# Performance work log

Hardware: AMD Instinct MI355X
Metric: run time of the kernel (lower is better)

Reference implementation:

```python
import jax, jax.numpy as jnp
import numpy as np
from jax import lax

NMS_THRESH = 0.5
BN_EPS = 1e-5
TO_REMOVE = 1.0  # neural-motifs box convention (+1 in width/height)


def nms_overlaps(boxes):
    # boxes: [N, C, 4] xyxy -> per-class pairwise IoU [N, N, C]
    x1 = jnp.maximum(boxes[:, None, :, 0], boxes[None, :, :, 0])
    y1 = jnp.maximum(boxes[:, None, :, 1], boxes[None, :, :, 1])
    x2 = jnp.minimum(boxes[:, None, :, 2], boxes[None, :, :, 2])
    y2 = jnp.minimum(boxes[:, None, :, 3], boxes[None, :, :, 3])
    inter = jnp.clip(x2 - x1 + TO_REMOVE, 0.0) * jnp.clip(y2 - y1 + TO_REMOVE, 0.0)
    area = (boxes[:, :, 2] - boxes[:, :, 0] + TO_REMOVE) * (boxes[:, :, 3] - boxes[:, :, 1] + TO_REMOVE)  # [N,C]
    union = area[:, None, :] + area[None, :, :] - inter
    return inter / union


def greedy_nms_labels(obj_dists, is_overlap):
    # faithful port of nms_per_cls: iterative argmax + per-class suppression
    N, C = obj_dists.shape
    scores = jax.nn.softmax(obj_dists, axis=-1)
    scores = scores.at[:, 0].set(-1.0)  # kill background column

    def step(carry, _):
        scores, labels = carry
        flat = jnp.argmax(scores)          # row-major, same as np.unravel_index
        box_ind = flat // C
        cls_ind = flat % C
        labels = labels.at[box_ind].set(cls_ind.astype(jnp.int32))
        ov = is_overlap[box_ind, :, cls_ind]  # [N] bool
        col = jnp.where(ov, 0.0, scores[:, cls_ind])
        scores = scores.at[:, cls_ind].set(col)
        scores = scores.at[box_ind, :].set(-1.0)
        return (scores, labels), None

    (_, labels), _ = lax.scan(step, (scores, jnp.zeros(N, jnp.int32)), None, length=N)
    return labels


def setup_inputs() -> dict:
    key = jax.random.key(0)
    ks = jax.random.split(key, 16)
    N, C, D, E, H, P = 400, 151, 4096, 200, 512, 128
    x = jax.random.normal(ks[0], (N, D), jnp.float32)
    predict_logits = jax.random.normal(ks[1], (N, C), jnp.float32) * 2.0
    pos_input = jax.random.uniform(ks[2], (N, 9), jnp.float32)
    xy = jax.random.uniform(ks[3], (N, C, 2), jnp.float32) * 800.0
    wh = jax.random.uniform(ks[4], (N, C, 2), jnp.float32) * 200.0 + 1.0
    boxes_per_cls = jnp.concatenate([xy, xy + wh], axis=-1)
    sc = lambda k, sh: jax.random.normal(k, sh, jnp.float32) * np.float32(1.0 / np.sqrt(sh[0]))
    return {
        'x': x,
        'predict_logits': predict_logits,
        'pos_input': pos_input,
        'boxes_per_cls': boxes_per_cls,
        'obj_embed_w': jax.random.normal(ks[5], (C, E), jnp.float32) * 0.1,
        'obj_embed2_w': jax.random.normal(ks[6], (C, E), jnp.float32) * 0.1,
        'w_pos1': sc(ks[7], (9, 32)), 'b_pos1': jnp.zeros(32, jnp.float32),
        'bn_gamma': jnp.ones(32, jnp.float32), 'bn_beta': jnp.zeros(32, jnp.float32),
        'bn_mean': jnp.zeros(32, jnp.float32), 'bn_var': jnp.ones(32, jnp.float32),
        'w_pos2': sc(ks[8], (32, P)), 'b_pos2': jnp.zeros(P, jnp.float32),
        'w_lin': sc(ks[9], (D + E + P, H)), 'b_lin': jnp.zeros(H, jnp.float32),
        'w_out': sc(ks[10], (H, C)), 'b_out': jnp.zeros(C, jnp.float32),
        'w_fc': sc(ks[11], (D + E + P, H)), 'b_fc': jnp.zeros(H, jnp.float32),
    }


def reference(x, predict_logits, pos_input, boxes_per_cls, obj_embed_w, obj_embed2_w,
              w_pos1, b_pos1, bn_gamma, bn_beta, bn_mean, bn_var, w_pos2, b_pos2,
              w_lin, b_lin, w_out, b_out, w_fc, b_fc):
    # sgdet inference path of VTransEFeaturePE.forward
    obj_embed = jax.nn.softmax(predict_logits, axis=-1) @ obj_embed_w           # [N,E]
    h = pos_input @ w_pos1 + b_pos1                                             # Linear(9,32)
    h = (h - bn_mean) / jnp.sqrt(bn_var + BN_EPS) * bn_gamma + bn_beta          # BN eval
    pos_embed = jax.nn.relu(h @ w_pos2 + b_pos2)                                # [N,128]
    rep = jnp.concatenate([x, obj_embed, pos_embed], axis=-1)                   # [N,4424]
    obj_dists = (rep @ w_lin + b_lin) @ w_out + b_out                           # [N,C]
    is_overlap = nms_overlaps(boxes_per_cls) >= NMS_THRESH                      # [N,N,C]
    obj_preds = greedy_nms_labels(obj_dists, is_overlap)                        # [N] int32
    obj_embed2 = obj_embed2_w[obj_preds]                                        # [N,E]
    obj_rel_rep = jnp.concatenate([x, pos_embed, obj_embed2], axis=-1)
    edge_ctx = jax.nn.relu(obj_rel_rep @ w_fc + b_fc)                           # [N,H]
    return (obj_dists, obj_preds, edge_ctx)
```

## Files before the change

kernel.cpp:

```cpp
#include <hip/hip_runtime.h>
#include <hip/hip_bf16.h>
#include <stdint.h>

#define NB 400
#define NC 151
#define DX 4096
#define DE 200
#define DP 128
#define DH 512
#define KREP 4424
#define TAILW 328
#define MPAD 416
#define SPLITK 8
#define TILES1 139
#define TILES2 132
#define SKSTRIDE 152

__device__ __forceinline__ uint32_t f2ord(float f) {
  uint32_t u = __float_as_uint(f);
  return (u & 0x80000000u) ? ~u : (u | 0x80000000u);
}

__global__ __launch_bounds__(256) void k_embed(
    const float* __restrict__ logits, const float* __restrict__ obj_embed_w,
    const float* __restrict__ pos_input, const float* __restrict__ w_pos1,
    const float* __restrict__ b_pos1, const float* __restrict__ bn_gamma,
    const float* __restrict__ bn_beta, const float* __restrict__ bn_mean,
    const float* __restrict__ bn_var, const float* __restrict__ w_pos2,
    const float* __restrict__ b_pos2, float* __restrict__ tail1) {
  int r = blockIdx.x, t = threadIdx.x;
  if (r >= NB) {
    if (t < TAILW) tail1[r * TAILW + t] = 0.f;
    return;
  }
  __shared__ float p[NC];
  __shared__ float red[256];
  __shared__ float hb[32];

  float v = (t < NC) ? logits[r * NC + t] : -INFINITY;
  red[t] = v; __syncthreads();
  for (int s = 128; s > 0; s >>= 1) { if (t < s) red[t] = fmaxf(red[t], red[t + s]); __syncthreads(); }
  float m = red[0]; __syncthreads();
  float e = (t < NC) ? expf(v - m) : 0.f;
  red[t] = e; __syncthreads();
  for (int s = 128; s > 0; s >>= 1) { if (t < s) red[t] += red[t + s]; __syncthreads(); }
  float sum = red[0];
  if (t < NC) p[t] = e / sum;

  if (t < 32) {
    float acc = b_pos1[t];
    for (int k = 0; k < 9; k++) acc += pos_input[r * 9 + k] * w_pos1[k * 32 + t];
    acc = (acc - bn_mean[t]) / sqrtf(bn_var[t] + 1e-5f) * bn_gamma[t] + bn_beta[t];
    hb[t] = acc;
  }
  __syncthreads();

  if (t < DE) {
    float acc = 0.f;
    for (int k = 0; k < NC; k++) acc += p[k] * obj_embed_w[k * DE + t];
    tail1[r * TAILW + t] = acc;
  }
  if (t < DP) {
    float acc = b_pos2[t];
    for (int k = 0; k < 32; k++) acc += hb[k] * w_pos2[k * DP + t];
    tail1[r * TAILW + DE + t] = fmaxf(acc, 0.f);
  }
}

__device__ __forceinline__ void gemm_body(
    float (*As)[36], float (*Bs)[68],
    const float* __restrict__ x, const float* __restrict__ tail,
    const float* __restrict__ w, float* __restrict__ part,
    int bid, int tiles, int toff) {
  int tid = threadIdx.x;
  int n0 = (bid & 7) * 64, m0 = ((bid >> 3) % 13) * 32;
  int z = bid / 104;
  int tbeg = (z * tiles) / SPLITK, tend = ((z + 1) * tiles) / SPLITK;
  int ty = tid >> 4, tx = tid & 15;
  int a_r = tid >> 3, a_c = (tid & 7) << 2;
  int b_r = tid >> 4, b_c = (tid & 15) << 2;
  float4 acc0 = {0, 0, 0, 0}, acc1 = {0, 0, 0, 0};

  auto loadA = [&](int t) -> float4 {
    int k = t * 32 + a_c;
    int row = m0 + a_r;
    float4 v = {0, 0, 0, 0};
    if (k < KREP) {
      if (k < DX) { if (row < NB) v = *(const float4*)&x[(size_t)row * DX + k]; }
      else v = *(const float4*)&tail[row * TAILW + toff + (k - DX)];
    }
    return v;
  };
  auto loadB = [&](int t, int roff) -> float4 {
    int k = t * 32 + b_r + roff;
    float4 v = {0, 0, 0, 0};
    if (k < KREP) v = *(const float4*)&w[(size_t)k * DH + n0 + b_c];
    return v;
  };

  float4 pa = loadA(tbeg), pb0 = loadB(tbeg, 0), pb1 = loadB(tbeg, 16);
  for (int t = tbeg; t < tend; t++) {
    __syncthreads();
    *(float4*)&As[a_r][a_c] = pa;
    *(float4*)&Bs[b_r][b_c] = pb0;
    *(float4*)&Bs[b_r + 16][b_c] = pb1;
    __syncthreads();
    if (t + 1 < tend) { pa = loadA(t + 1); pb0 = loadB(t + 1, 0); pb1 = loadB(t + 1, 16); }
#pragma unroll
    for (int k4 = 0; k4 < 8; k4++) {
      float4 a0 = *(float4*)&As[ty * 2][k4 * 4];
      float4 a1 = *(float4*)&As[ty * 2 + 1][k4 * 4];
#pragma unroll
      for (int j = 0; j < 4; j++) {
        float4 bv = *(float4*)&Bs[k4 * 4 + j][tx * 4];
        float av0 = (&a0.x)[j], av1 = (&a1.x)[j];
        acc0.x += av0 * bv.x; acc0.y += av0 * bv.y; acc0.z += av0 * bv.z; acc0.w += av0 * bv.w;
        acc1.x += av1 * bv.x; acc1.y += av1 * bv.y; acc1.z += av1 * bv.z; acc1.w += av1 * bv.w;
      }
    }
  }
  int row0 = m0 + ty * 2, col = n0 + tx * 4;
  float* base = part + (size_t)z * NB * DH;
  if (row0 < NB)     *(float4*)&base[row0 * DH + col] = acc0;
  if (row0 + 1 < NB) *(float4*)&base[(row0 + 1) * DH + col] = acc1;
}

__global__ __launch_bounds__(256) void k_g1ov(
    const float* __restrict__ x, const float* __restrict__ tail1,
    const float* __restrict__ w_lin, float* __restrict__ part,
    const float* __restrict__ boxes, uint64_t* __restrict__ ov_bits) {
  __shared__ __align__(16) float As[32][36];
  __shared__ __align__(16) float Bs[32][68];
  int bid = blockIdx.x;
  if (bid >= 832) {
    int c = bid - 832;
    int t = threadIdx.x;
    __shared__ float4 bx[NB];
    const float4* bp4 = (const float4*)boxes;
    for (int j = t; j < NB; j += 256) bx[j] = bp4[j * NC + c];
    __syncthreads();
    int wave = t >> 6, lane = t & 63;
    for (int b = wave; b < NB; b += 4) {
      float4 A = bx[b];
      float areaA = (A.z - A.x + 1.f) * (A.w - A.y + 1.f);
      for (int chunk = 0; chunk < 7; chunk++) {
        int j = chunk * 64 + lane;
        bool ov = false;
        if (j < NB) {
          float4 B = bx[j];
          float x1 = fmaxf(A.x, B.x), y1 = fmaxf(A.y, B.y);
          float x2 = fminf(A.z, B.z), y2 = fminf(A.w, B.w);
          float iw = fmaxf(x2 - x1 + 1.f, 0.f), ih = fmaxf(y2 - y1 + 1.f, 0.f);
          float inter = iw * ih;
          float areaB = (B.z - B.x + 1.f) * (B.w - B.y + 1.f);
          ov = (inter / (areaA + areaB - inter)) >= 0.5f;
        }
        uint64_t mask = __ballot(ov);
        if (lane == 0) ov_bits[((size_t)(b * NC + c) << 3) + chunk] = mask;
      }
    }
    return;
  }
  gemm_body(As, Bs, x, tail1, w_lin, part, bid, TILES1, 0);
}

__global__ __launch_bounds__(256) void k_dists(
    const float* __restrict__ part, const float* __restrict__ b_lin,
    const float* __restrict__ w_out, const float* __restrict__ b_out,
    float* __restrict__ out_dists, uint64_t* __restrict__ skeys) {
  int r = blockIdx.x, t = threadIdx.x;
  __shared__ float h[DH];
  __shared__ float red[256];
  __shared__ float sval[NC];
  float s0 = b_lin[t], s1 = b_lin[t + 256];
#pragma unroll
  for (int z = 0; z < SPLITK; z++) {
    const float* pr = part + ((size_t)z * NB + r) * DH;
    s0 += pr[t]; s1 += pr[t + 256];
  }
  h[t] = s0; h[t + 256] = s1;
  __syncthreads();

  float acc = -INFINITY;
  if (t < NC) {
    acc = b_out[t];
    for (int k = 0; k < DH; k++) acc += h[k] * w_out[k * NC + t];
    out_dists[r * NC + t] = acc;
  }
  red[t] = (t < NC) ? acc : -INFINITY; __syncthreads();
  for (int s = 128; s > 0; s >>= 1) { if (t < s) red[t] = fmaxf(red[t], red[t + s]); __syncthreads(); }
  float mx = red[0]; __syncthreads();
  float e = (t < NC) ? expf(acc - mx) : 0.f;
  red[t] = e; __syncthreads();
  for (int s = 128; s > 0; s >>= 1) { if (t < s) red[t] += red[t + s]; __syncthreads(); }
  float sum = red[0];
  if (t < NC) sval[t] = e / sum;
  __syncthreads();

  if (t >= 1 && t < NC) {
    float v = sval[t];
    int rank = 0;
    for (int c2 = 1; c2 < NC; c2++) {
      float v2 = sval[c2];
      rank += (v2 > v) || (v2 == v && c2 < t);
    }
    skeys[(size_t)r * SKSTRIDE + rank] =
        ((uint64_t)f2ord(v) << 17) | ((uint64_t)(511 - r) << 8) | (uint64_t)t;
  }
}

struct GemmSm { float As[32][36]; float Bs[32][68]; };
struct NmsSm  { uint64_t top4[2][4][4]; uint64_t amask[8]; uint64_t rmask[8];
                uint32_t rcol32[512]; uint64_t ovc[NB][8]; };

__global__ __launch_bounds__(256) void k_nms_g2a(
    const uint64_t* __restrict__ ov_bits, const uint64_t* __restrict__ skeys,
    int* __restrict__ labels_g, float* __restrict__ out_preds,
    const float* __restrict__ x, const float* __restrict__ tail1,
    const float* __restrict__ w_fc, float* __restrict__ part) {
  __shared__ __align__(16) union { GemmSm g; NmsSm n; } sm;
  if (blockIdx.x > 0) {
    gemm_body(sm.g.As, sm.g.Bs, x, tail1, w_fc, part, blockIdx.x - 1, TILES2, DE);
    return;
  }
  int tid = threadIdx.x, wave = tid >> 6, lane = tid & 63;
  int S0w = wave * 2;
  uint64_t cand[2];
  uint64_t supp0[2], supp1[2], supp2[2];
  int depth[2];
  bool removed[2];
  int reszmin[2];

#pragma unroll
  for (int u = 0; u < 2; u++) {
    int r = (S0w + u) * 64 + lane;
    supp0[u] = supp1[u] = supp2[u] = 0;
    depth[u] = 0; removed[u] = false; reszmin[u] = 255;
    if (r < NB) {
      cand[u] = skeys[(size_t)r * SKSTRIDE];
      labels_g[r] = 0; out_preds[r] = 0.f;
    } else cand[u] = 0;
  }

  auto cswap = [](uint64_t& a, uint64_t& b) {
    uint64_t hi = a > b ? a : b, lo = a > b ? b : a; a = hi; b = lo;
  };

  int picked = 0, rr = 0;
  while (picked < NB) {
    int pp = rr & 1; rr++;
    uint64_t k0 = cand[0] > cand[1] ? cand[0] : cand[1];
    uint64_t k1 = cand[0] > cand[1] ? cand[1] : cand[0];
    uint64_t k2 = 0, k3 = 0;
#pragma unroll
    for (int off = 1; off < 64; off <<= 1) {
      uint64_t p0 = (uint64_t)__shfl_xor((unsigned long long)k0, off, 64);
      uint64_t p1 = (uint64_t)__shfl_xor((unsigned long long)k1, off, 64);
      uint64_t p2 = (uint64_t)__shfl_xor((unsigned long long)k2, off, 64);
      uint64_t p3 = (uint64_t)__shfl_xor((unsigned long long)k3, off, 64);
      uint64_t t0 = k0 > p3 ? k0 : p3;
      uint64_t t1 = k1 > p2 ? k1 : p2;
      uint64_t t2 = k2 > p1 ? k2 : p1;
      uint64_t t3 = k3 > p0 ? k3 : p0;
      cswap(t0, t2); cswap(t1, t3); cswap(t0, t1); cswap(t2, t3);
      k0 = t0; k1 = t1; k2 = t2; k3 = t3;
    }
    if (lane < 4) {
      uint64_t kv = (lane == 0) ? k0 : (lane == 1) ? k1 : (lane == 2) ? k2 : k3;
      sm.n.top4[pp][wave][lane] = kv;
    }
    __syncthreads();

    uint64_t A0 = sm.n.top4[pp][0][0], A1 = sm.n.top4[pp][0][1], A2 = sm.n.top4[pp][0][2], A3 = sm.n.top4[pp][0][3];
    uint64_t B0 = sm.n.top4[pp][1][0], B1 = sm.n.top4[pp][1][1], B2 = sm.n.top4[pp][1][2], B3 = sm.n.top4[pp][1][3];
    uint64_t C0 = sm.n.top4[pp][2][0], C1 = sm.n.top4[pp][2][1], C2 = sm.n.top4[pp][2][2], C3 = sm.n.top4[pp][2][3];
    uint64_t D0 = sm.n.top4[pp][3][0], D1 = sm.n.top4[pp][3][1], D2 = sm.n.top4[pp][3][2], D3 = sm.n.top4[pp][3][3];
    uint64_t x0 = A0, x1 = A1, x2 = A2, x3 = A3, x4 = B3, x5 = B2, x6 = B1, x7 = B0;
    cswap(x0,x4); cswap(x1,x5); cswap(x2,x6); cswap(x3,x7);
    cswap(x0,x2); cswap(x1,x3); cswap(x4,x6); cswap(x5,x7);
    cswap(x0,x1); cswap(x2,x3); cswap(x4,x5); cswap(x6,x7);
    uint64_t y0 = C0, y1 = C1, y2 = C2, y3 = C3, y4 = D3, y5 = D2, y6 = D1, y7 = D0;
    cswap(y0,y4); cswap(y1,y5); cswap(y2,y6); cswap(y3,y7);
    cswap(y0,y2); cswap(y1,y3); cswap(y4,y6); cswap(y5,y7);
    cswap(y0,y1); cswap(y2,y3); cswap(y4,y5); cswap(y6,y7);
    uint64_t tk[8];
    tk[0] = x0 > y7 ? x0 : y7;  tk[1] = x1 > y6 ? x1 : y6;
    tk[2] = x2 > y5 ? x2 : y5;  tk[3] = x3 > y4 ? x3 : y4;
    tk[4] = x4 > y3 ? x4 : y3;  tk[5] = x5 > y2 ? x5 : y2;
    tk[6] = x6 > y1 ? x6 : y1;  tk[7] = x7 > y0 ? x7 : y0;
    cswap(tk[0],tk[4]); cswap(tk[1],tk[5]); cswap(tk[2],tk[6]); cswap(tk[3],tk[7]);
    cswap(tk[0],tk[2]); cswap(tk[1],tk[3]); cswap(tk[4],tk[6]); cswap(tk[5],tk[7]);
    cswap(tk[0],tk[1]); cswap(tk[2],tk[3]); cswap(tk[4],tk[5]); cswap(tk[6],tk[7]);

    if ((uint32_t)(tk[0] >> 17) <= 0x80000000u) break;

    int cntA = 0, cntB = 0, cntC = 0, cntD = 0;
#pragma unroll
    for (int i = 0; i < 8; i++) {
      cntA += (tk[i] > A3); cntB += (tk[i] > B3);
      cntC += (tk[i] > C3); cntD += (tk[i] > D3);
    }
    int mincnt = cntA < cntB ? cntA : cntB;
    mincnt = mincnt < cntC ? mincnt : cntC;
    mincnt = mincnt < cntD ? mincnt : cntD;

    int npick = NB - picked; if (npick > 8) npick = 8;

    int pi = lane >> 3, pw = lane & 7;
    int bsel = 0, csel = 0;
#pragma unroll
    for (int i = 0; i < 8; i++)
      if (pi == i) {
        bsel = 511 - (int)((tk[i] >> 8) & 0x1FF);
        csel = (int)(tk[i] & 0xFF);
      }
    uint64_t wv = 0;
    if (pi < npick && pw < 7)
      wv = ov_bits[(((size_t)(bsel * NC + csel)) << 3) + pw];
    uint32_t packed = ((uint32_t)bsel << 8) | (uint32_t)csel;

    uint64_t balnz_raw = __ballot(wv != 0ull);

    uint64_t ovall = 0;
#pragma unroll
    for (int j = 0; j < 8; j++) {
      int bj = 511 - (int)((tk[j] >> 8) & 0x1FF);
      bool hit = (pw == (bj >> 6)) && ((wv >> (bj & 63)) & 1);
      uint64_t bal = __ballot(hit);
      bal |= bal >> 4; bal |= bal >> 2; bal |= bal >> 1;
      uint32_t m8 = (uint32_t)(((bal & 0x0101010101010101ULL) * 0x0102040810204080ULL) >> 56);
      ovall |= (uint64_t)m8 << (8 * j);
    }

    int napply = 1; bool stop = false;
#pragma unroll
    for (int j = 1; j < 8; j++) {
      bool bad = (j >= npick) || (j > mincnt) ||
                 ((uint32_t)(tk[j] >> 17) <= 0x80000000u);
      int cjv = (int)(tk[j] & 0xFF);
#pragma unroll
      for (int i = 0; i < j; i++)
        bad = bad || (((int)(tk[i] & 0xFF) == cjv) && ((ovall >> (8 * j + i)) & 1));
      stop = stop || bad;
      if (!stop) napply = j + 1;
    }

    uint64_t am = (napply >= 8) ? ~0ull : ((1ull << (8 * napply)) - 1);
    uint64_t balnz = balnz_raw & am;

#pragma unroll
    for (int u = 0; u < 2; u++) {
      int S = S0w + u;
      int r = S * 64 + lane;
      for (int i = 0; i < napply; i++) {
        int bc = __shfl((int)packed, i * 8, 64);
        int b = (bc >> 8) & 0x1FF, c = bc & 0xFF;
        bool act = ((balnz >> (i * 8 + S)) & 1) || ((b >> 6) == S);
        if (!act) continue;
        uint64_t owv = (uint64_t)__shfl((unsigned long long)wv, i * 8 + S, 64);
        if (r == b) {
          removed[u] = true; reszmin[u] = 255;
          cand[u] = ((uint64_t)0x407FFFFFu << 17) | ((uint64_t)(511 - r) << 8);
          labels_g[b] = c; out_preds[b] = (float)c;
        } else if ((owv >> lane) & 1) {
          if (removed[u]) {
            if (c < reszmin[u]) reszmin[u] = c;
            cand[u] = ((uint64_t)0x80000000u << 17) | ((uint64_t)(511 - r) << 8)
                      | (uint64_t)reszmin[u];
          } else {
            uint64_t bit = 1ull << (c & 63);
            if (c < 64) supp0[u] |= bit; else if (c < 128) supp1[u] |= bit; else supp2[u] |= bit;
            if ((int)(cand[u] & 0xFF) == c) {
              int d = depth[u] + 1;
              uint64_t k = 0;
              for (; d < 150; d++) {
                k = skeys[(size_t)r * SKSTRIDE + d];
                int col = (int)(k & 0xFF);
                uint64_t mm = (col < 64) ? supp0[u] : ((col < 128) ? supp1[u] : supp2[u]);
                if (!((mm >> (col & 63)) & 1)) break;
              }
              if (d >= 150)
                k = ((uint64_t)0x80000000u << 17) | ((uint64_t)(511 - r) << 8) | 1ull;
              depth[u] = d; cand[u] = k;
            }
          }
        }
      }
    }
    picked += napply;
  }

  if (picked < NB) {
#pragma unroll
    for (int u = 0; u < 2; u++) {
      int r = (S0w + u) * 64 + lane;
      uint64_t am = __ballot(r < NB && !removed[u]);
      uint64_t rm = __ballot(removed[u] &&
                             (uint32_t)(cand[u] >> 17) == 0x80000000u);
      sm.n.rcol32[(S0w + u) * 64 + lane] = (uint32_t)reszmin[u];
      if (lane == 0) { sm.n.amask[S0w + u] = am; sm.n.rmask[S0w + u] = rm; }
    }
    __syncthreads();
    for (int i = tid; i < NB * 8; i += 256) {
      int r = i >> 3, w = i & 7;
      sm.n.ovc[r][w] = (w < 7) ? ov_bits[(((size_t)(r * NC + 1)) << 3) + w] : 0;
    }
    __syncthreads();
    for (int r = tid; r < NB; r += 256) {
      if ((sm.n.rmask[r >> 6] >> (r & 63)) & 1ull) {
        uint32_t c = sm.n.rcol32[r];
        for (int w = 0; w < 7; w++)
          sm.n.ovc[r][w] = ov_bits[(((size_t)(r * NC + (int)c)) << 3) + w];
      }
    }
    __syncthreads();
    if (wave != 0) return;

    uint64_t A[8], R[8];
#pragma unroll
    for (int s = 0; s < 8; s++) { A[s] = sm.n.amask[s]; R[s] = sm.n.rmask[s]; }

    while (picked < NB) {
      int b = 0, sstar = 0; bool found = false;
#pragma unroll
      for (int s = 0; s < 8; s++) {
        uint64_t cm = A[s] | R[s];
        if (!found && cm != 0ull) {
          found = true; sstar = s;
          b = s * 64 + (int)__builtin_ctzll(cm);
        }
      }
      bool fromA = false;
#pragma unroll
      for (int s = 0; s < 8; s++)
        if (s == sstar) fromA = (A[s] >> (b & 63)) & 1ull;
      if (!found) fromA = false;
      uint32_t colv = 0;
      if (found) colv = fromA ? 1u : sm.n.rcol32[b];

      uint64_t W[8];
      if (found) {
#pragma unroll
        for (int s = 0; s < 7; s++) W[s] = sm.n.ovc[b][s];
        W[7] = 0;
      } else {
        uint64_t w = 0;
        if (lane < 7) w = ov_bits[(((size_t)(b * NC + (int)colv)) << 3) + lane];
#pragma unroll
        for (int s = 0; s < 8; s++)
          W[s] = (uint64_t)__shfl((unsigned long long)w, s, 64);
      }
      uint64_t T[8];
#pragma unroll
      for (int s = 0; s < 8; s++) {
        uint64_t valid = (s < 6) ? ~0ull : ((s == 6) ? 0xFFFFull : 0ull);
        T[s] = W[s] & valid & ~A[s];
      }
#pragma unroll
      for (int s = 0; s < 8; s++)
        if (s == sstar) {
          T[s] &= ~(1ull << (b & 63));
          if (found) {
            if (fromA) A[s] &= ~(1ull << (b & 63));
            else       R[s] &= ~(1ull << (b & 63));
          }
        }
      if (found && !fromA) {
        if (lane == 0) sm.n.rcol32[b] = 255;
      }
#pragma unroll
      for (int s = 0; s < 8; s++) R[s] |= T[s];

#pragma unroll
      for (int s = 0; s < 8; s++) {
        uint64_t tt = T[s];
        while (tt) {
          int bit = (int)__builtin_ctzll(tt); tt &= tt - 1;
          int row = s * 64 + bit;
          uint32_t rcv = sm.n.rcol32[row];
          if (rcv > colv) {
            if (lane == 0) sm.n.rcol32[row] = colv;
            uint64_t w2 = 0;
            if (lane < 7) {
              w2 = ov_bits[(((size_t)(row * NC + (int)colv)) << 3) + lane];
              sm.n.ovc[row][lane] = w2;
            }
          }
        }
      }
      if (lane == 0) { labels_g[b] = (int)colv; out_preds[b] = (float)colv; }
      picked++;
    }
  }
}

__global__ __launch_bounds__(256) void k_final(
    const float* __restrict__ emb2, const int* __restrict__ labels,
    const float* __restrict__ w_fc, const float* __restrict__ part,
    const float* __restrict__ b_fc, float* __restrict__ out_edge) {
  __shared__ __align__(16) float As[32][36];
  __shared__ __align__(16) float Bs[32][68];
  int tid = threadIdx.x;
  int n0 = blockIdx.x * 64, m0 = blockIdx.y * 32;
  int ty = tid >> 4, tx = tid & 15;
  int a_r = tid >> 3, a_c = (tid & 7) << 2;
  int b_r = tid >> 4, b_c = (tid & 15) << 2;
  float4 acc0 = {0, 0, 0, 0}, acc1 = {0, 0, 0, 0};
  int row_a = m0 + a_r;
  int lab = (row_a < NB) ? labels[row_a] : 0;

  auto loadA = [&](int t) -> float4 {
    int kk = t * 32 + a_c;
    float4 v = {0, 0, 0, 0};
    if (kk < DE && row_a < NB) v = *(const float4*)&emb2[(size_t)lab * DE + kk];
    return v;
  };
  auto loadB = [&](int t, int roff) -> float4 {
    int kk = t * 32 + b_r + roff;
    float4 v = {0, 0, 0, 0};
    if (kk < DE) v = *(const float4*)&w_fc[(size_t)(DX + DP + kk) * DH + n0 + b_c];
    return v;
  };

  float4 pa = loadA(0), pb0 = loadB(0, 0), pb1 = loadB(0, 16);
  for (int t = 0; t < 7; t++) {
    __syncthreads();
    *(float4*)&As[a_r][a_c] = pa;
    *(float4*)&Bs[b_r][b_c] = pb0;
    *(float4*)&Bs[b_r + 16][b_c] = pb1;
    __syncthreads();
    if (t + 1 < 7) { pa = loadA(t + 1); pb0 = loadB(t + 1, 0); pb1 = loadB(t + 1, 16); }
#pragma unroll
    for (int k4 = 0; k4 < 8; k4++) {
      float4 a0 = *(float4*)&As[ty * 2][k4 * 4];
      float4 a1 = *(float4*)&As[ty * 2 + 1][k4 * 4];
#pragma unroll
      for (int j = 0; j < 4; j++) {
        float4 bv = *(float4*)&Bs[k4 * 4 + j][tx * 4];
        float av0 = (&a0.x)[j], av1 = (&a1.x)[j];
        acc0.x += av0 * bv.x; acc0.y += av0 * bv.y; acc0.z += av0 * bv.z; acc0.w += av0 * bv.w;
        acc1.x += av1 * bv.x; acc1.y += av1 * bv.y; acc1.z += av1 * bv.z; acc1.w += av1 * bv.w;
      }
    }
  }
  int row0 = m0 + ty * 2, col = n0 + tx * 4;
#pragma unroll
  for (int z = 0; z < SPLITK; z++) {
    if (row0 < NB) {
      float4 p = *(const float4*)&part[((size_t)z * NB + row0) * DH + col];
      acc0.x += p.x; acc0.y += p.y; acc0.z += p.z; acc0.w += p.w;
    }
    if (row0 + 1 < NB) {
      float4 p = *(const float4*)&part[((size_t)z * NB + row0 + 1) * DH + col];
      acc1.x += p.x; acc1.y += p.y; acc1.z += p.z; acc1.w += p.w;
    }
  }
  float4 bv = *(const float4*)&b_fc[col];
  if (row0 < NB) {
    float4 r;
    r.x = fmaxf(acc0.x + bv.x, 0.f); r.y = fmaxf(acc0.y + bv.y, 0.f);
    r.z = fmaxf(acc0.z + bv.z, 0.f); r.w = fmaxf(acc0.w + bv.w, 0.f);
    *(float4*)&out_edge[row0 * DH + col] = r;
  }
  if (row0 + 1 < NB) {
    float4 r;
    r.x = fmaxf(acc1.x + bv.x, 0.f); r.y = fmaxf(acc1.y + bv.y, 0.f);
    r.z = fmaxf(acc1.z + bv.z, 0.f); r.w = fmaxf(acc1.w + bv.w, 0.f);
    *(float4*)&out_edge[(row0 + 1) * DH + col] = r;
  }
}

extern "C" void kernel_launch(void* const* d_in, const int* in_sizes, int n_in,
                              void* d_out, int out_size, void* d_ws, size_t ws_size,
                              hipStream_t stream) {
  const float* x            = (const float*)d_in[0];
  const float* logits       = (const float*)d_in[1];
  const float* pos_input    = (const float*)d_in[2];
  const float* boxes        = (const float*)d_in[3];
  const float* obj_embed_w  = (const float*)d_in[4];
  const float* obj_embed2_w = (const float*)d_in[5];
  const float* w_pos1       = (const float*)d_in[6];
  const float* b_pos1       = (const float*)d_in[7];
  const float* bn_gamma     = (const float*)d_in[8];
  const float* bn_beta      = (const float*)d_in[9];
  const float* bn_mean      = (const float*)d_in[10];
  const float* bn_var       = (const float*)d_in[11];
  const float* w_pos2       = (const float*)d_in[12];
  const float* b_pos2       = (const float*)d_in[13];
  const float* w_lin        = (const float*)d_in[14];
  const float* b_lin        = (const float*)d_in[15];
  const float* w_out        = (const float*)d_in[16];
  const float* b_out        = (const float*)d_in[17];
  const float* w_fc         = (const float*)d_in[18];
  const float* b_fc         = (const float*)d_in[19];

  float* ws         = (float*)d_ws;
  float* tail1      = ws;
  int* labels       = (int*)(tail1 + MPAD * TAILW);
  uint64_t* skeys   = (uint64_t*)(labels + MPAD);
  uint64_t* ov_bits = skeys + (size_t)NB * SKSTRIDE;
  float* part       = (float*)(ov_bits + (size_t)NB * NC * 8);

  float* out       = (float*)d_out;
  float* out_dists = out;
  float* out_preds = out + NB * NC;
  float* out_edge  = out + NB * NC + NB;

  k_embed<<<MPAD, 256, 0, stream>>>(logits, obj_embed_w, pos_input, w_pos1, b_pos1,
                                    bn_gamma, bn_beta, bn_mean, bn_var, w_pos2, b_pos2,
                                    tail1);
  k_g1ov<<<983, 256, 0, stream>>>(x, tail1, w_lin, part, boxes, ov_bits);
  k_dists<<<NB, 256, 0, stream>>>(part, b_lin, w_out, b_out, out_dists, skeys);
  k_nms_g2a<<<833, 256, 0, stream>>>(ov_bits, skeys, labels, out_preds,
                                     x, tail1, w_fc, part);
  k_final<<<dim3(8, 13), 256, 0, stream>>>(obj_embed2_w, labels, w_fc, part,
                                           b_fc, out_edge);
}
```

Before: 567.5 us.

## Shrink NMS batch to top-4 and reuse previous round's overlap rows

The greedy NMS loop now merges the per-wave top-4 lists into a global top-4 with bitonic merges instead of a global top-8, and drops the mincnt check. It caches the previous round's candidate keys and overlap-bit rows and fetches them with a wave shuffle instead of reloading from global memory when a candidate reappears. The aim is to cut merge-network work and global-load latency per round. The cost is that at most 4 picks are applied per iteration, which may raise the number of barrier-synchronized rounds. Dropping the mincnt check may also affect correctness, since a global top-4 built from per-wave top-4 lists is always exact but picks past them were previously guarded.

```diff
diff --git a/kernel.cpp b/kernel.cpp
--- a/kernel.cpp
+++ b/kernel.cpp
@@ -245,8 +245,21 @@
   auto cswap = [](uint64_t& a, uint64_t& b) {
     uint64_t hi = a > b ? a : b, lo = a > b ? b : a; a = hi; b = lo;
   };
+  auto merge4 = [&](uint64_t a0, uint64_t a1, uint64_t a2, uint64_t a3,
+                    uint64_t e0, uint64_t e1, uint64_t e2, uint64_t e3,
+                    uint64_t& o0, uint64_t& o1, uint64_t& o2, uint64_t& o3) {
+    uint64_t m0 = a0 > e3 ? a0 : e3;
+    uint64_t m1 = a1 > e2 ? a1 : e2;
+    uint64_t m2 = a2 > e1 ? a2 : e1;
+    uint64_t m3 = a3 > e0 ? a3 : e0;
+    cswap(m0, m2); cswap(m1, m3); cswap(m0, m1); cswap(m2, m3);
+    o0 = m0; o1 = m1; o2 = m2; o3 = m3;
+  };
 
   int picked = 0, rr = 0;
+  uint64_t ptk0 = 0, ptk1 = 0, ptk2 = 0, ptk3 = 0;
+  uint64_t pwv = 0;
+  int pnp = 0;
   while (picked < NB) {
     int pp = rr & 1; rr++;
     uint64_t k0 = cand[0] > cand[1] ? cand[0] : cand[1];
@@ -275,47 +288,29 @@
     uint64_t B0 = sm.n.top4[pp][1][0], B1 = sm.n.top4[pp][1][1], B2 = sm.n.top4[pp][1][2], B3 = sm.n.top4[pp][1][3];
     uint64_t C0 = sm.n.top4[pp][2][0], C1 = sm.n.top4[pp][2][1], C2 = sm.n.top4[pp][2][2], C3 = sm.n.top4[pp][2][3];
     uint64_t D0 = sm.n.top4[pp][3][0], D1 = sm.n.top4[pp][3][1], D2 = sm.n.top4[pp][3][2], D3 = sm.n.top4[pp][3][3];
-    uint64_t x0 = A0, x1 = A1, x2 = A2, x3 = A3, x4 = B3, x5 = B2, x6 = B1, x7 = B0;
-    cswap(x0,x4); cswap(x1,x5); cswap(x2,x6); cswap(x3,x7);
-    cswap(x0,x2); cswap(x1,x3); cswap(x4,x6); cswap(x5,x7);
-    cswap(x0,x1); cswap(x2,x3); cswap(x4,x5); cswap(x6,x7);
-    uint64_t y0 = C0, y1 = C1, y2 = C2, y3 = C3, y4 = D3, y5 = D2, y6 = D1, y7 = D0;
-    cswap(y0,y4); cswap(y1,y5); cswap(y2,y6); cswap(y3,y7);
-    cswap(y0,y2); cswap(y1,y3); cswap(y4,y6); cswap(y5,y7);
-    cswap(y0,y1); cswap(y2,y3); cswap(y4,y5); cswap(y6,y7);
-    uint64_t tk[8];
-    tk[0] = x0 > y7 ? x0 : y7;  tk[1] = x1 > y6 ? x1 : y6;
-    tk[2] = x2 > y5 ? x2 : y5;  tk[3] = x3 > y4 ? x3 : y4;
-    tk[4] = x4 > y3 ? x4 : y3;  tk[5] = x5 > y2 ? x5 : y2;
-    tk[6] = x6 > y1 ? x6 : y1;  tk[7] = x7 > y0 ? x7 : y0;
-    cswap(tk[0],tk[4]); cswap(tk[1],tk[5]); cswap(tk[2],tk[6]); cswap(tk[3],tk[7]);
-    cswap(tk[0],tk[2]); cswap(tk[1],tk[3]); cswap(tk[4],tk[6]); cswap(tk[5],tk[7]);
-    cswap(tk[0],tk[1]); cswap(tk[2],tk[3]); cswap(tk[4],tk[5]); cswap(tk[6],tk[7]);
-
-    if ((uint32_t)(tk[0] >> 17) <= 0x80000000u) break;
-
-    int cntA = 0, cntB = 0, cntC = 0, cntD = 0;
-#pragma unroll
-    for (int i = 0; i < 8; i++) {
-      cntA += (tk[i] > A3); cntB += (tk[i] > B3);
-      cntC += (tk[i] > C3); cntD += (tk[i] > D3);
-    }
-    int mincnt = cntA < cntB ? cntA : cntB;
-    mincnt = mincnt < cntC ? mincnt : cntC;
-    mincnt = mincnt < cntD ? mincnt : cntD;
-
-    int npick = NB - picked; if (npick > 8) npick = 8;
+    uint64_t P0, P1, P2, P3, Q0, Q1, Q2, Q3, g0, g1, g2, g3;
+    merge4(A0, A1, A2, A3, B0, B1, B2, B3, P0, P1, P2, P3);
+    merge4(C0, C1, C2, C3, D0, D1, D2, D3, Q0, Q1, Q2, Q3);
+    merge4(P0, P1, P2, P3, Q0, Q1, Q2, Q3, g0, g1, g2, g3);
+
+    if ((uint32_t)(g0 >> 17) <= 0x80000000u) break;
+
+    int npick = NB - picked; if (npick > 4) npick = 4;
 
     int pi = lane >> 3, pw = lane & 7;
-    int bsel = 0, csel = 0;
-#pragma unroll
-    for (int i = 0; i < 8; i++)
-      if (pi == i) {
-        bsel = 511 - (int)((tk[i] >> 8) & 0x1FF);
-        csel = (int)(tk[i] & 0xFF);
-      }
+    uint64_t gj = (pi == 0) ? g0 : (pi == 1) ? g1 : (pi == 2) ? g2 : g3;
+    int bsel = 511 - (int)((gj >> 8) & 0x1FF);
+    int csel = (int)(gj & 0xFF);
+    int src = (gj == ptk0) ? 0 : (gj == ptk1) ? 1 : (gj == ptk2) ? 2
+            : (gj == ptk3) ? 3 : -1;
+    if (src >= pnp) src = -1;
     uint64_t wv = 0;
-    if (pi < npick && pw < 7)
+    {
+      int idx = (src >= 0 ? src : 0) * 8 + pw;
+      uint64_t ru = (uint64_t)__shfl((unsigned long long)pwv, idx, 64);
+      if (src >= 0 && pi < npick && pw < 7) wv = ru;
+    }
+    if (src < 0 && pi < npick && pw < 7)
       wv = ov_bits[(((size_t)(bsel * NC + csel)) << 3) + pw];
     uint32_t packed = ((uint32_t)bsel << 8) | (uint32_t)csel;
 
@@ -323,8 +318,11 @@
 
     uint64_t ovall = 0;
 #pragma unroll
-    for (int j = 0; j < 8; j++) {
-      int bj = 511 - (int)((tk[j] >> 8) & 0x1FF);
+    for (int j = 0; j < 4; j++) {
+      int bj = (j == 0) ? (511 - (int)((g0 >> 8) & 0x1FF))
+             : (j == 1) ? (511 - (int)((g1 >> 8) & 0x1FF))
+             : (j == 2) ? (511 - (int)((g2 >> 8) & 0x1FF))
+             :            (511 - (int)((g3 >> 8) & 0x1FF));
       bool hit = (pw == (bj >> 6)) && ((wv >> (bj & 63)) & 1);
       uint64_t bal = __ballot(hit);
       bal |= bal >> 4; bal |= bal >> 2; bal |= bal >> 1;
@@ -334,18 +332,20 @@
 
     int napply = 1; bool stop = false;
 #pragma unroll
-    for (int j = 1; j < 8; j++) {
-      bool bad = (j >= npick) || (j > mincnt) ||
-                 ((uint32_t)(tk[j] >> 17) <= 0x80000000u);
-      int cjv = (int)(tk[j] & 0xFF);
-#pragma unroll
-      for (int i = 0; i < j; i++)
-        bad = bad || (((int)(tk[i] & 0xFF) == cjv) && ((ovall >> (8 * j + i)) & 1));
+    for (int j = 1; j < 4; j++) {
+      uint64_t gjj = (j == 1) ? g1 : (j == 2) ? g2 : g3;
+      bool bad = (j >= npick) || ((uint32_t)(gjj >> 17) <= 0x80000000u);
+      int cjv = (int)(gjj & 0xFF);
+#pragma unroll
+      for (int i = 0; i < j; i++) {
+        uint64_t gii = (i == 0) ? g0 : (i == 1) ? g1 : (i == 2) ? g2 : g3;
+        bad = bad || (((int)(gii & 0xFF) == cjv) && ((ovall >> (8 * j + i)) & 1));
+      }
       stop = stop || bad;
       if (!stop) napply = j + 1;
     }
 
-    uint64_t am = (napply >= 8) ? ~0ull : ((1ull << (8 * napply)) - 1);
+    uint64_t am = (1ull << (8 * napply)) - 1;
     uint64_t balnz = balnz_raw & am;
 
 #pragma unroll
@@ -387,6 +387,8 @@
         }
       }
     }
+    ptk0 = g0; ptk1 = g1; ptk2 = g2; ptk3 = g3;
+    pwv = wv; pnp = npick;
     picked += napply;
   }
 
```

Measured after the change: 627.3 us. +10.5%, slower.
